# Optimization experiments

Measured on AMD Instinct MI355X. Metric: run time of the kernel, lower is better.

The kernel has to match this reference:

```python
import jax, jax.numpy as jnp
import numpy as np

B, S, H, J, LAT, OBS = 256, 128, 1024, 12, 64, 51
NL = 13                  # fk_model link count
PD = (NL + 1) * 3        # pos_dim = 42
FPS = 30.0
ACT_SCALE = 0.25
SMIN, SMAX = 0.05, 0.5
PIN = 2 * J + OBS + LAT  # 139


def setup_inputs() -> dict:
    key = jax.random.key(0)
    ks = jax.random.split(key, 16)
    rn = lambda k, shape, s=0.02: jax.random.normal(k, shape, dtype=jnp.float32) * s
    return dict(
        z=jax.random.normal(ks[0], (B, LAT), jnp.float32),
        obs_seq=jax.random.normal(ks[1], (B, S, OBS), jnp.float32),
        W1=rn(ks[2], (H, PIN)), b1=jnp.zeros((H,), jnp.float32),
        g1=jnp.ones((H,), jnp.float32), be1=jnp.zeros((H,), jnp.float32),
        W2=rn(ks[3], (H, H)), b2=jnp.zeros((H,), jnp.float32),
        g2=jnp.ones((H,), jnp.float32), be2=jnp.zeros((H,), jnp.float32),
        Wa1=rn(ks[4], (H, H)), ba1=jnp.zeros((H,), jnp.float32),
        Wa2=rn(ks[5], (J, H)), ba2=jnp.zeros((J,), jnp.float32),
        Wo=rn(ks[6], (3, H)), bo=jnp.zeros((3,), jnp.float32),
        Wv=rn(ks[7], (PD, H)), bv=jnp.full((PD,), -2.0, jnp.float32),  # torch init: zeros weight, bias=-2 (we keep small random W for non-degenerate grads)
        alpha_logits=jnp.full((J,), float(np.log(0.3)), jnp.float32),
        fk_W=rn(ks[8], (NL * 3, J), 0.1), fk_b=rn(ks[9], (NL * 3,), 0.1),  # linear FK surrogate
        pos_mean=rn(ks[10], (NL + 1, 3), 0.1),
        pos_std=1.0 + jax.random.uniform(ks[11], (NL + 1, 3), jnp.float32),
        joint_lower=jnp.full((J,), -2.0, jnp.float32),
        joint_upper=jnp.full((J,), 2.0, jnp.float32),
        default_dof_pos=rn(ks[12], (J,), 0.3),
    )


def _layernorm(x, g, b):
    m = jnp.mean(x, axis=-1, keepdims=True)
    v = jnp.var(x, axis=-1, keepdims=True)
    return (x - m) * jax.lax.rsqrt(v + 1e-5) * g + b


def reference(z, obs_seq, W1, b1, g1, be1, W2, b2, g2, be2, Wa1, ba1, Wa2, ba2,
              Wo, bo, Wv, bv, alpha_logits, fk_W, fk_b, pos_mean, pos_std,
              joint_lower, joint_upper, default_dof_pos):
    j_range = (joint_upper - joint_lower) / 2.0
    j_mean = (joint_upper + joint_lower) / 2.0
    alpha = jax.nn.sigmoid(alpha_logits)
    Bsz = z.shape[0]

    def step(carry, obs_t):
        pj, pdq = carry                                 # [B,J] each
        jn = (pj - j_mean) / j_range
        x = jnp.concatenate([jn, pdq, obs_t, z], axis=-1)   # [B,PIN]
        h = jax.nn.relu(_layernorm(x @ W1.T + b1, g1, be1))
        h = jax.nn.relu(_layernorm(h @ W2.T + b2, g2, be2))  # [B,H]
        a = jnp.tanh(jax.nn.relu(h @ Wa1.T + ba1) @ Wa2.T + ba2)  # [B,J]
        tgt = a * ACT_SCALE + default_dof_pos
        cj = jnp.clip(pj + alpha * (tgt - pj), joint_lower, joint_upper)
        obj = h @ Wo.T + bo                             # [B,3]
        # torch detaches the carried state (prev_joints/prev_dq)
        cdq = (cj - pj) * FPS
        new_carry = (jax.lax.stop_gradient(cj), jax.lax.stop_gradient(cdq))
        return new_carry, (h, a, cj, obj)

    pj0 = jnp.broadcast_to(default_dof_pos, (Bsz, J))
    pdq0 = jnp.zeros((Bsz, J), z.dtype)
    _, (hs, acts, joints, objs) = jax.lax.scan(step, (pj0, pdq0), jnp.swapaxes(obs_seq, 0, 1))

    features_seq = jnp.swapaxes(hs, 0, 1)    # [B,S,H]
    actions_seq = jnp.swapaxes(acts, 0, 1)   # [B,S,J]
    joint_traj = jnp.swapaxes(joints, 0, 1)  # [B,S,J]
    object_traj = jnp.swapaxes(objs, 0, 1)   # [B,S,3]

    agent_traj = joint_traj @ fk_W.T + fk_b  # [B,S,NL*3] linear FK surrogate
    combined = jnp.concatenate([agent_traj, object_traj], axis=-1)
    combined = combined.reshape(Bsz, S, NL + 1, 3)
    graph_x_mu = ((combined - pos_mean) / pos_std).reshape(Bsz, S, -1)  # [B,S,PD]

    sigma = SMIN + (SMAX - SMIN) * jax.nn.sigmoid(features_seq @ Wv.T + bv)
    log_sigma_pos = jnp.log(sigma)           # [B,S,PD]
    return (graph_x_mu, joint_traj, actions_seq, log_sigma_pos)
```

## Files before the change

kernel.cpp:

```cpp
#include <hip/hip_runtime.h>
#include <math.h>


#define NB 256
#define NS 128
#define NH 1024
#define NJ 12
#define NPIN 139
#define NPD 42
#define WPG 32
#define BROW 32
#define W2S 1032
#define AS 1032

typedef __attribute__((ext_vector_type(8))) short short8;
typedef __attribute__((ext_vector_type(4))) float f32x4;
typedef __attribute__((ext_vector_type(4))) unsigned short u16x4;

struct Params {
  const float* z; const float* obs; const float* W1; const float* b1;
  const float* g1; const float* be1; const float* W2; const float* b2;
  const float* g2; const float* be2; const float* Wa1; const float* ba1;
  const float* Wa2; const float* ba2; const float* Wo; const float* bo;
  const float* Wv; const float* bv; const float* alog; const float* fkW;
  const float* fkb; const float* pmean; const float* pstd; const float* jlo;
  const float* jhi; const float* ddp;
  float* out_gmu; float* out_joint; float* out_act; float* out_ls;
  float* zc; float* pa;
  unsigned short* y1b; unsigned short* y2b;
  unsigned short* wa1b; unsigned short* wexb;
  unsigned int* gcnt; unsigned int* slots;
};

__device__ __forceinline__ unsigned short f2bf(float x) {
  union { float f; unsigned u; } v; v.f = x;
  unsigned r = v.u + 0x7FFFu + ((v.u >> 16) & 1u);
  return (unsigned short)(r >> 16);
}
__device__ __forceinline__ float bf2f(unsigned short x) {
  union { unsigned u; float f; } v; v.u = ((unsigned)x) << 16;
  return v.f;
}
__device__ __forceinline__ unsigned cvt_pk_bf16(float lo, float hi) {
  unsigned r;
  asm("v_cvt_pk_bf16_f32 %0, %1, %2" : "=v"(r) : "v"(lo), "v"(hi));
  return r;
}
__device__ __forceinline__ void ld16_sc0(const unsigned short* p, short8& d) {
  asm volatile("global_load_dwordx4 %0, %1, off sc0" : "=v"(d) : "v"(p));
}
__device__ __forceinline__ void ldf4_sc0(const float* p, f32x4& d) {
  asm volatile("global_load_dwordx4 %0, %1, off sc0" : "=v"(d) : "v"(p));
}
__device__ __forceinline__ void vwait0() {
  asm volatile("s_waitcnt vmcnt(0)" ::: "memory");
  __builtin_amdgcn_sched_barrier(0);
}

__device__ __forceinline__ f32x4 dot1024(const unsigned short* a, const unsigned short* b) {
  const short8* ap = (const short8*)a;
  const short8* bp = (const short8*)b;
  f32x4 acc0 = {0.f, 0.f, 0.f, 0.f};
  f32x4 acc1 = {0.f, 0.f, 0.f, 0.f};
#pragma unroll 4
  for (int k8 = 0; k8 < 128; k8 += 8) {
    acc0 = __builtin_amdgcn_mfma_f32_16x16x32_bf16(ap[k8], bp[k8], acc0, 0, 0, 0);
    acc1 = __builtin_amdgcn_mfma_f32_16x16x32_bf16(ap[k8 + 4], bp[k8 + 4], acc1, 0, 0, 0);
  }
  return acc0 + acc1;
}

__device__ __forceinline__ void gbar(unsigned int* c, unsigned int target) {
  __threadfence();
  __syncthreads();
  if (threadIdx.x == 0) {
    __hip_atomic_fetch_add(c, 1u, __ATOMIC_RELEASE, __HIP_MEMORY_SCOPE_AGENT);
    unsigned long long t0 = __builtin_amdgcn_s_memrealtime();
    while (__hip_atomic_load(c, __ATOMIC_ACQUIRE, __HIP_MEMORY_SCOPE_AGENT) < target) {
      __builtin_amdgcn_s_sleep(16);
      if (__builtin_amdgcn_s_memrealtime() - t0 > (1ull << 25)) break;
    }
  }
  __syncthreads();
  __threadfence();
}

__device__ __forceinline__ void xbar2(unsigned int* sg, int w, unsigned target,
                                      int wave, int lane) {
  asm volatile("s_waitcnt vmcnt(0)" ::: "memory");
  __syncthreads();
  if (wave == 0) {
    if (lane == 0)
      __hip_atomic_fetch_add(sg + (size_t)w * 16, 1u, __ATOMIC_RELAXED,
                             __HIP_MEMORY_SCOPE_AGENT);
    const unsigned int* myslot = sg + (size_t)(lane & 31) * 16;
    unsigned long long t0 = __builtin_amdgcn_s_memrealtime();
    for (;;) {
      unsigned v;
      asm volatile("global_load_dword %0, %1, off sc0 sc1\n\t"
                   "s_waitcnt vmcnt(0)"
                   : "=v"(v) : "v"(myslot) : "memory");
      if (__all(v >= target)) break;
      __builtin_amdgcn_s_sleep(1);
      if (__builtin_amdgcn_s_memrealtime() - t0 > (1ull << 23)) break;
    }
  }
  __syncthreads();
}

__global__ __launch_bounds__(256, 1) void decoder_persistent(Params p) {
  __shared__ unsigned short w2l[BROW * W2S];
  __shared__ unsigned short albuf[BROW * AS];
  __shared__ float g1l[NH], be1l[NH], g2l[NH], be2l[NH];
  __shared__ unsigned short t1l[BROW * 40];
  __shared__ unsigned short wa2l[16 * 40];
  __shared__ float pj_l[BROW * NJ], pdq_l[BROW * NJ];
  __shared__ float alpha_l[NJ], jm_l[NJ], jri_l[NJ], lo_l[NJ], hi_l[NJ], ddp_l[NJ], ba2_l[NJ];
  __shared__ float pm_l[NPD], psi_l[NPD], bv_l[NPD], bo_l[4];

  const int tid = threadIdx.x;
  const int bid = blockIdx.x;
  const int g = bid & 7;
  const int w = bid >> 3;
  const int b0 = g * BROW;
  const int n0 = w * 32;
  const int wave = tid >> 6;
  const int lane = tid & 63;

  unsigned int* sg = p.slots + (size_t)g * 512;
  unsigned short* y1bg = p.y1b + (size_t)g * BROW * NH;
  unsigned short* y2bg = p.y2b + (size_t)g * BROW * NH;
  float* pa_gg = p.pa + (size_t)g * BROW * NJ * 32;

  if (tid < NJ) {
    alpha_l[tid] = 1.f / (1.f + expf(-p.alog[tid]));
    float lo = p.jlo[tid], hi = p.jhi[tid];
    jm_l[tid] = 0.5f * (hi + lo);
    jri_l[tid] = 2.f / (hi - lo);
    lo_l[tid] = lo; hi_l[tid] = hi;
    ddp_l[tid] = p.ddp[tid]; ba2_l[tid] = p.ba2[tid];
  }
  if (tid < NPD) { pm_l[tid] = p.pmean[tid]; psi_l[tid] = 1.f / p.pstd[tid]; bv_l[tid] = p.bv[tid]; }
  if (tid < 3) bo_l[tid] = p.bo[tid];
  for (int idx = tid; idx < BROW * NJ; idx += 256) { pj_l[idx] = p.ddp[idx % NJ]; pdq_l[idx] = 0.f; }
  for (int idx = tid; idx < NH; idx += 256) {
    g1l[idx] = p.g1[idx]; be1l[idx] = p.be1[idx];
    g2l[idx] = p.g2[idx]; be2l[idx] = p.be2[idx];
  }
  for (int idx = tid; idx < BROW * NH; idx += 256) {
    int r = idx >> 10, k = idx & (NH - 1);
    w2l[r * W2S + k] = f2bf(p.W2[(size_t)(n0 + r) * NH + k]);
  }
  for (int idx = tid; idx < 16 * 32; idx += 256) {
    int rr = idx >> 5, cc = idx & 31;
    wa2l[rr * 40 + cc] = (rr < NJ) ? f2bf(p.Wa2[(size_t)rr * NH + n0 + cc]) : (unsigned short)0;
  }
  {
    int r = tid >> 3, cq = tid & 7;
    int nb = n0 + cq * 4;
    const float* zr = p.z + (size_t)(b0 + r) * 64;
    const float* w1r = p.W1 + (size_t)nb * NPIN + 75;
    float a0 = p.b1[nb], a1 = p.b1[nb + 1], a2 = p.b1[nb + 2], a3 = p.b1[nb + 3];
    for (int k = 0; k < 64; ++k) {
      float zv = zr[k];
      a0 += zv * w1r[k]; a1 += zv * w1r[NPIN + k];
      a2 += zv * w1r[2 * NPIN + k]; a3 += zv * w1r[3 * NPIN + k];
    }
    f32x4 st = {a0, a1, a2, a3};
    *(f32x4*)(p.zc + (size_t)(b0 + r) * NH + nb) = st;
  }
  for (int idx = tid; idx < 4 * NH; idx += 256) {
    int r = idx >> 10, k = idx & (NH - 1);
    int row = n0 + g * 4 + r;
    p.wa1b[(size_t)row * NH + k] = f2bf(p.Wa1[(size_t)row * NH + k]);
  }
  if (bid == 1) {
    for (int idx = tid; idx < 48 * NH; idx += 256) {
      int r = idx >> 10, k = idx & (NH - 1);
      unsigned short v = 0;
      if (r < 3) v = f2bf(p.Wo[(size_t)r * NH + k]);
      else if (r < 45) v = f2bf(p.Wv[(size_t)(r - 3) * NH + k]);
      p.wexb[idx] = v;
    }
  }
  gbar(p.gcnt, 256u);

  auto stage_ln = [&](const unsigned short* yg, const float* gl, const float* bl) {
    const int r = tid >> 3, cq = tid & 7;
    const unsigned short* src = yg + (size_t)r * NH + cq * 8;
    unsigned short* dst = &albuf[r * AS + cq * 8];
    short8 v[16];
#pragma unroll
    for (int i = 0; i < 16; ++i) ld16_sc0(src + (size_t)i * 64, v[i]);
    vwait0();
    float s = 0.f, q = 0.f;
#pragma unroll
    for (int i = 0; i < 16; ++i)
#pragma unroll
      for (int jj = 0; jj < 8; ++jj) {
        float x = bf2f((unsigned short)v[i][jj]);
        s += x; q = fmaf(x, x, q);
      }
#pragma unroll
    for (int off = 4; off; off >>= 1) {
      s += __shfl_down(s, off, 8);
      q += __shfl_down(q, off, 8);
    }
    s = __shfl(s, 0, 8); q = __shfl(q, 0, 8);
    float m = s * (1.f / 1024.f);
    float rs = rsqrtf(q * (1.f / 1024.f) - m * m + 1e-5f);
    float nmrs = -m * rs;
#pragma unroll
    for (int i = 0; i < 16; ++i) {
      int c = cq * 8 + i * 64;
      f32x4 ga = *(const f32x4*)(gl + c);
      f32x4 gb = *(const f32x4*)(gl + c + 4);
      f32x4 ba = *(const f32x4*)(bl + c);
      f32x4 bb = *(const f32x4*)(bl + c + 4);
      float xn[8];
#pragma unroll
      for (int jj = 0; jj < 8; ++jj) {
        float x = bf2f((unsigned short)v[i][jj]);
        float tn = fmaf(x, rs, nmrs);
        float gg = (jj < 4) ? ga[jj] : gb[jj - 4];
        float bv2 = (jj < 4) ? ba[jj] : bb[jj - 4];
        xn[jj] = fmaxf(fmaf(tn, gg, bv2), 0.f);
      }
      uint4 pk = {cvt_pk_bf16(xn[0], xn[1]), cvt_pk_bf16(xn[2], xn[3]),
                  cvt_pk_bf16(xn[4], xn[5]), cvt_pk_bf16(xn[6], xn[7])};
      *(uint4*)(dst + i * 64) = pk;
    }
  };

  auto P1 = [&](int t) {
    int r = tid >> 3, cq = tid & 7;
    int nb = n0 + cq * 4;
    float xj[24];
#pragma unroll
    for (int j = 0; j < NJ; ++j) {
      xj[j] = (pj_l[r * NJ + j] - jm_l[j]) * jri_l[j];
      xj[12 + j] = pdq_l[r * NJ + j];
    }
    f32x4 acc = *(const f32x4*)(p.zc + (size_t)(b0 + r) * NH + nb);
    const float* w1r = p.W1 + (size_t)nb * NPIN;
#pragma unroll
    for (int k = 0; k < 24; ++k) {
      float xv = xj[k];
      acc[0] += xv * w1r[k]; acc[1] += xv * w1r[NPIN + k];
      acc[2] += xv * w1r[2 * NPIN + k]; acc[3] += xv * w1r[3 * NPIN + k];
    }
    const float* ob = p.obs + ((size_t)(b0 + r) * NS + t) * 51;
    for (int o = 0; o < 51; ++o) {
      float ov = ob[o];
      acc[0] += ov * w1r[24 + o]; acc[1] += ov * w1r[NPIN + 24 + o];
      acc[2] += ov * w1r[2 * NPIN + 24 + o]; acc[3] += ov * w1r[3 * NPIN + 24 + o];
    }
    u16x4 hv = {f2bf(acc[0]), f2bf(acc[1]), f2bf(acc[2]), f2bf(acc[3])};
    *(u16x4*)(y1bg + (size_t)r * NH + nb) = hv;
  };

  auto Yphase = [&]() {
    stage_ln(y1bg, g1l, be1l);
    __syncthreads();
    int rt = wave >> 1, ct = wave & 1;
    int kq = (lane >> 4) * 8;
    const unsigned short* a = &albuf[(rt * 16 + (lane & 15)) * AS + kq];
    const unsigned short* b = &w2l[(ct * 16 + (lane & 15)) * W2S + kq];
    f32x4 acc = dot1024(a, b);
    int col = n0 + ct * 16 + (lane & 15);
    float b2v = p.b2[col];
#pragma unroll
    for (int i = 0; i < 4; ++i) {
      int row = rt * 16 + (lane >> 4) * 4 + i;
      y2bg[(size_t)row * NH + col] = f2bf(acc[i] + b2v);
    }
  };

  auto Zphase = [&](int t) {
    stage_ln(y2bg, g2l, be2l);
    __syncthreads();
    int rt = wave >> 1, ct = wave & 1;
    int kq = (lane >> 4) * 8;
    {
      const unsigned short* a = &albuf[(rt * 16 + (lane & 15)) * AS + kq];
      const unsigned short* b = p.wa1b + (size_t)(n0 + ct * 16 + (lane & 15)) * NH + kq;
      f32x4 acc = dot1024(a, b);
      int lcol = ct * 16 + (lane & 15);
      float bav = p.ba1[n0 + lcol];
#pragma unroll
      for (int i = 0; i < 4; ++i) {
        int row = rt * 16 + (lane >> 4) * 4 + i;
        t1l[row * 40 + lcol] = f2bf(fmaxf(acc[i] + bav, 0.f));
      }
    }
    __syncthreads();
    if (wave < 2) {
      int k0 = (lane >> 4) * 8;
      short8 a8 = *(const short8*)&t1l[(wave * 16 + (lane & 15)) * 40 + k0];
      short8 b8 = *(const short8*)&wa2l[(lane & 15) * 40 + k0];
      f32x4 z4 = {0.f, 0.f, 0.f, 0.f};
      f32x4 d = __builtin_amdgcn_mfma_f32_16x16x32_bf16(a8, b8, z4, 0, 0, 0);
      int j = lane & 15;
      if (j < NJ) {
#pragma unroll
        for (int i = 0; i < 4; ++i) {
          int row = wave * 16 + (lane >> 4) * 4 + i;
          pa_gg[((size_t)row * NJ + j) * 32 + w] = d[i];
        }
      }
    }
    if (w >= 26 && wave == 3) {
      int e = w - 26, cte = e >> 1, rte = e & 1;
      const unsigned short* a = &albuf[(rte * 16 + (lane & 15)) * AS + kq];
      const unsigned short* b = p.wexb + (size_t)(cte * 16 + (lane & 15)) * NH + kq;
      f32x4 acc = dot1024(a, b);
      int ec = cte * 16 + (lane & 15);
#pragma unroll
      for (int i = 0; i < 4; ++i) {
        int row = rte * 16 + (lane >> 4) * 4 + i;
        int bb = b0 + row;
        if (ec < 3) {
          float val = acc[i] + bo_l[ec];
          p.out_gmu[((size_t)bb * NS + t) * NPD + 39 + ec] = (val - pm_l[39 + ec]) * psi_l[39 + ec];
        } else if (ec < 45) {
          int sv = ec - 3;
          float val = acc[i] + bv_l[sv];
          float sig = 0.05f + 0.45f / (1.f + expf(-val));
          p.out_ls[((size_t)bb * NS + t) * NPD + sv] = logf(sig);
        }
      }
    }
  };

  auto Xmid = [&](int tp) {
    for (int e = tid; e < BROW * NJ; e += 256) {
      const float* pp = pa_gg + (size_t)e * 32;
      f32x4 u[8];
#pragma unroll
      for (int c2 = 0; c2 < 8; ++c2) ldf4_sc0(pp + c2 * 4, u[c2]);
      vwait0();
      f32x4 ss = ((u[0] + u[1]) + (u[2] + u[3])) + ((u[4] + u[5]) + (u[6] + u[7]));
      float sum = ss[0] + ss[1] + ss[2] + ss[3];
      int r = e / NJ, j = e - r * NJ;
      float av = tanhf(sum + ba2_l[j]);
      float pj = pj_l[e];
      float tgt = av * 0.25f + ddp_l[j];
      float cj = pj + alpha_l[j] * (tgt - pj);
      cj = fminf(fmaxf(cj, lo_l[j]), hi_l[j]);
      pdq_l[e] = (cj - pj) * 30.f;
      pj_l[e] = cj;
      if (w == 0) {
        size_t o = ((size_t)(b0 + r) * NS + tp) * NJ + j;
        p.out_joint[o] = cj;
        p.out_act[o] = av;
      }
    }
    __syncthreads();
    if (w == 0) {
      for (int idx = tid; idx < BROW * 39; idx += 256) {
        int r = idx / 39, m = idx - r * 39;
        float s = p.fkb[m];
        const float* fw = p.fkW + m * NJ;
#pragma unroll
        for (int j = 0; j < NJ; ++j) s += pj_l[r * NJ + j] * fw[j];
        p.out_gmu[((size_t)(b0 + r) * NS + tp) * NPD + m] = (s - pm_l[m]) * psi_l[m];
      }
    }
  };

  unsigned int nbar = 0;
  for (int t = 0; t < NS; ++t) {
    if (t > 0) Xmid(t - 1);
    P1(t);
    xbar2(sg, w, ++nbar, wave, lane);
    Yphase();
    xbar2(sg, w, ++nbar, wave, lane);
    Zphase(t);
    xbar2(sg, w, ++nbar, wave, lane);
  }
  Xmid(NS - 1);
}

extern "C" void kernel_launch(void* const* d_in, const int* in_sizes, int n_in,
                              void* d_out, int out_size, void* d_ws, size_t ws_size,
                              hipStream_t stream) {
  (void)in_sizes; (void)n_in; (void)out_size; (void)ws_size;
  char* ws = (char*)d_ws;
  Params p;
  p.z = (const float*)d_in[0];   p.obs = (const float*)d_in[1];
  p.W1 = (const float*)d_in[2];  p.b1 = (const float*)d_in[3];
  p.g1 = (const float*)d_in[4];  p.be1 = (const float*)d_in[5];
  p.W2 = (const float*)d_in[6];  p.b2 = (const float*)d_in[7];
  p.g2 = (const float*)d_in[8];  p.be2 = (const float*)d_in[9];
  p.Wa1 = (const float*)d_in[10]; p.ba1 = (const float*)d_in[11];
  p.Wa2 = (const float*)d_in[12]; p.ba2 = (const float*)d_in[13];
  p.Wo = (const float*)d_in[14]; p.bo = (const float*)d_in[15];
  p.Wv = (const float*)d_in[16]; p.bv = (const float*)d_in[17];
  p.alog = (const float*)d_in[18];
  p.fkW = (const float*)d_in[19]; p.fkb = (const float*)d_in[20];
  p.pmean = (const float*)d_in[21]; p.pstd = (const float*)d_in[22];
  p.jlo = (const float*)d_in[23]; p.jhi = (const float*)d_in[24];
  p.ddp = (const float*)d_in[25];

  float* out = (float*)d_out;
  p.out_gmu = out;
  p.out_joint = out + (size_t)256 * 128 * 42;
  p.out_act = p.out_joint + (size_t)256 * 128 * 12;
  p.out_ls = p.out_act + (size_t)256 * 128 * 12;

  p.gcnt = (unsigned int*)(ws + 0);
  p.slots = (unsigned int*)(ws + 1024);
  size_t off = (size_t)1 << 15;
  p.zc = (float*)(ws + off);                 off += (size_t)NB * NH * 4;
  p.y1b = (unsigned short*)(ws + off);       off += (size_t)NB * NH * 2;
  p.y2b = (unsigned short*)(ws + off);       off += (size_t)NB * NH * 2;
  p.pa = (float*)(ws + off);                 off += (size_t)8 * 32 * 12 * 32 * 4;
  p.wa1b = (unsigned short*)(ws + off);      off += (size_t)NH * NH * 2;
  p.wexb = (unsigned short*)(ws + off);

  hipMemsetAsync(d_ws, 0, 1 << 15, stream);
  decoder_persistent<<<dim3(256), dim3(256), 0, stream>>>(p);
}
```

Baseline: 3.873 ms.

## Fuse LayerNorm partial stats into producers and overlap obs projection with barrier

Producers of y1 and y2 now compute per-row partial sums and sums of squares and write them to small global buffers. The LayerNorm staging then reduces these partials instead of re-reading every bf16 value for the statistics. The loop is also restructured so the observation part of the first-layer projection for the next step is issued between the barrier arrive and the wait, hiding it behind synchronisation latency. The cost is extra global writes and reads of partials and a more intricate barrier schedule. Statistics are computed from fp32 values before bf16 rounding, which changes numerics slightly.

```diff
diff --git a/kernel.cpp b/kernel.cpp
--- a/kernel.cpp
+++ b/kernel.cpp
@@ -26,7 +26,7 @@
   const float* fkb; const float* pmean; const float* pstd; const float* jlo;
   const float* jhi; const float* ddp;
   float* out_gmu; float* out_joint; float* out_act; float* out_ls;
-  float* zc; float* pa;
+  float* zc; float* pa; float* part1; float* part2;
   unsigned short* y1b; unsigned short* y2b;
   unsigned short* wa1b; unsigned short* wexb;
   unsigned int* gcnt; unsigned int* slots;
@@ -85,6 +85,20 @@
   __threadfence();
 }
 
+__device__ __forceinline__ void slot_wait(unsigned int* sg, unsigned target, int lane) {
+  const unsigned int* myslot = sg + (size_t)(lane & 31) * 16;
+  unsigned long long t0 = __builtin_amdgcn_s_memrealtime();
+  for (;;) {
+    unsigned v;
+    asm volatile("global_load_dword %0, %1, off sc0 sc1\n\t"
+                 "s_waitcnt vmcnt(0)"
+                 : "=v"(v) : "v"(myslot) : "memory");
+    if (__all(v >= target)) break;
+    __builtin_amdgcn_s_sleep(1);
+    if (__builtin_amdgcn_s_memrealtime() - t0 > (1ull << 23)) break;
+  }
+}
+
 __device__ __forceinline__ void xbar2(unsigned int* sg, int w, unsigned target,
                                       int wave, int lane) {
   asm volatile("s_waitcnt vmcnt(0)" ::: "memory");
@@ -93,17 +107,7 @@
     if (lane == 0)
       __hip_atomic_fetch_add(sg + (size_t)w * 16, 1u, __ATOMIC_RELAXED,
                              __HIP_MEMORY_SCOPE_AGENT);
-    const unsigned int* myslot = sg + (size_t)(lane & 31) * 16;
-    unsigned long long t0 = __builtin_amdgcn_s_memrealtime();
-    for (;;) {
-      unsigned v;
-      asm volatile("global_load_dword %0, %1, off sc0 sc1\n\t"
-                   "s_waitcnt vmcnt(0)"
-                   : "=v"(v) : "v"(myslot) : "memory");
-      if (__all(v >= target)) break;
-      __builtin_amdgcn_s_sleep(1);
-      if (__builtin_amdgcn_s_memrealtime() - t0 > (1ull << 23)) break;
-    }
+    slot_wait(sg, target, lane);
   }
   __syncthreads();
 }
@@ -131,6 +135,8 @@
   unsigned short* y1bg = p.y1b + (size_t)g * BROW * NH;
   unsigned short* y2bg = p.y2b + (size_t)g * BROW * NH;
   float* pa_gg = p.pa + (size_t)g * BROW * NJ * 32;
+  float* part1g = p.part1 + (size_t)g * BROW * 64;
+  float* part2g = p.part2 + (size_t)g * BROW * 128;
 
   if (tid < NJ) {
     alpha_l[tid] = 1.f / (1.f + expf(-p.alog[tid]));
@@ -185,22 +191,27 @@
   }
   gbar(p.gcnt, 256u);
 
-  auto stage_ln = [&](const unsigned short* yg, const float* gl, const float* bl) {
+  auto stage_ln_apply = [&](const unsigned short* yg, const float* part, bool wide,
+                            const float* gl, const float* bl) {
     const int r = tid >> 3, cq = tid & 7;
     const unsigned short* src = yg + (size_t)r * NH + cq * 8;
     unsigned short* dst = &albuf[r * AS + cq * 8];
     short8 v[16];
 #pragma unroll
     for (int i = 0; i < 16; ++i) ld16_sc0(src + (size_t)i * 64, v[i]);
+    const int fpr = wide ? 128 : 64;
+    const float* pp = part + (size_t)r * fpr + cq * (fpr >> 3);
+    f32x4 p0, p1, p2 = {0, 0, 0, 0}, p3 = {0, 0, 0, 0};
+    ldf4_sc0(pp, p0);
+    ldf4_sc0(pp + 4, p1);
+    if (wide) { ldf4_sc0(pp + 8, p2); ldf4_sc0(pp + 12, p3); }
     vwait0();
-    float s = 0.f, q = 0.f;
-#pragma unroll
-    for (int i = 0; i < 16; ++i)
-#pragma unroll
-      for (int jj = 0; jj < 8; ++jj) {
-        float x = bf2f((unsigned short)v[i][jj]);
-        s += x; q = fmaf(x, x, q);
-      }
+    float s = p0[0] + p0[2] + p1[0] + p1[2];
+    float q = p0[1] + p0[3] + p1[1] + p1[3];
+    if (wide) {
+      s += p2[0] + p2[2] + p3[0] + p3[2];
+      q += p2[1] + p2[3] + p3[1] + p3[3];
+    }
 #pragma unroll
     for (int off = 4; off; off >>= 1) {
       s += __shfl_down(s, off, 8);
@@ -232,35 +243,52 @@
     }
   };
 
-  auto P1 = [&](int t) {
+  auto P1_obs = [&](int t) -> f32x4 {
     int r = tid >> 3, cq = tid & 7;
     int nb = n0 + cq * 4;
-    float xj[24];
-#pragma unroll
-    for (int j = 0; j < NJ; ++j) {
-      xj[j] = (pj_l[r * NJ + j] - jm_l[j]) * jri_l[j];
-      xj[12 + j] = pdq_l[r * NJ + j];
-    }
     f32x4 acc = *(const f32x4*)(p.zc + (size_t)(b0 + r) * NH + nb);
     const float* w1r = p.W1 + (size_t)nb * NPIN;
-#pragma unroll
-    for (int k = 0; k < 24; ++k) {
-      float xv = xj[k];
-      acc[0] += xv * w1r[k]; acc[1] += xv * w1r[NPIN + k];
-      acc[2] += xv * w1r[2 * NPIN + k]; acc[3] += xv * w1r[3 * NPIN + k];
-    }
     const float* ob = p.obs + ((size_t)(b0 + r) * NS + t) * 51;
     for (int o = 0; o < 51; ++o) {
       float ov = ob[o];
       acc[0] += ov * w1r[24 + o]; acc[1] += ov * w1r[NPIN + 24 + o];
       acc[2] += ov * w1r[2 * NPIN + 24 + o]; acc[3] += ov * w1r[3 * NPIN + 24 + o];
     }
+    return acc;
+  };
+  auto P1_fin = [&](f32x4 acc) {
+    int r = tid >> 3, cq = tid & 7;
+    int nb = n0 + cq * 4;
+    float xj[24];
+#pragma unroll
+    for (int j = 0; j < NJ; ++j) {
+      xj[j] = (pj_l[r * NJ + j] - jm_l[j]) * jri_l[j];
+      xj[12 + j] = pdq_l[r * NJ + j];
+    }
+    const float* w1r = p.W1 + (size_t)nb * NPIN;
+#pragma unroll
+    for (int k = 0; k < 24; ++k) {
+      float xv = xj[k];
+      acc[0] += xv * w1r[k]; acc[1] += xv * w1r[NPIN + k];
+      acc[2] += xv * w1r[2 * NPIN + k]; acc[3] += xv * w1r[3 * NPIN + k];
+    }
     u16x4 hv = {f2bf(acc[0]), f2bf(acc[1]), f2bf(acc[2]), f2bf(acc[3])};
     *(u16x4*)(y1bg + (size_t)r * NH + nb) = hv;
+    float s = acc[0] + acc[1] + acc[2] + acc[3];
+    float q = acc[0] * acc[0] + acc[1] * acc[1] + acc[2] * acc[2] + acc[3] * acc[3];
+#pragma unroll
+    for (int off = 4; off; off >>= 1) {
+      s += __shfl_down(s, off, 8);
+      q += __shfl_down(q, off, 8);
+    }
+    if ((tid & 7) == 0) {
+      float* pw = part1g + (size_t)r * 64 + w * 2;
+      pw[0] = s; pw[1] = q;
+    }
   };
 
   auto Yphase = [&]() {
-    stage_ln(y1bg, g1l, be1l);
+    stage_ln_apply(y1bg, part1g, false, g1l, be1l);
     __syncthreads();
     int rt = wave >> 1, ct = wave & 1;
     int kq = (lane >> 4) * 8;
@@ -269,15 +297,34 @@
     f32x4 acc = dot1024(a, b);
     int col = n0 + ct * 16 + (lane & 15);
     float b2v = p.b2[col];
+    float sv[4], qv[4];
 #pragma unroll
     for (int i = 0; i < 4; ++i) {
       int row = rt * 16 + (lane >> 4) * 4 + i;
-      y2bg[(size_t)row * NH + col] = f2bf(acc[i] + b2v);
+      float val = acc[i] + b2v;
+      y2bg[(size_t)row * NH + col] = f2bf(val);
+      sv[i] = val; qv[i] = val * val;
+    }
+#pragma unroll
+    for (int mask = 1; mask < 16; mask <<= 1) {
+#pragma unroll
+      for (int i = 0; i < 4; ++i) {
+        sv[i] += __shfl_xor(sv[i], mask, 64);
+        qv[i] += __shfl_xor(qv[i], mask, 64);
+      }
+    }
+    if ((lane & 15) == 0) {
+      int rbase = rt * 16 + (lane >> 4) * 4;
+#pragma unroll
+      for (int i = 0; i < 4; ++i) {
+        float* pw = part2g + (size_t)(rbase + i) * 128 + (w * 2 + ct) * 2;
+        pw[0] = sv[i]; pw[1] = qv[i];
+      }
     }
   };
 
   auto Zphase = [&](int t) {
-    stage_ln(y2bg, g2l, be2l);
+    stage_ln_apply(y2bg, part2g, true, g2l, be2l);
     __syncthreads();
     int rt = wave >> 1, ct = wave & 1;
     int kq = (lane >> 4) * 8;
@@ -323,10 +370,10 @@
           float val = acc[i] + bo_l[ec];
           p.out_gmu[((size_t)bb * NS + t) * NPD + 39 + ec] = (val - pm_l[39 + ec]) * psi_l[39 + ec];
         } else if (ec < 45) {
-          int sv = ec - 3;
-          float val = acc[i] + bv_l[sv];
+          int sv2 = ec - 3;
+          float val = acc[i] + bv_l[sv2];
           float sig = 0.05f + 0.45f / (1.f + expf(-val));
-          p.out_ls[((size_t)bb * NS + t) * NPD + sv] = logf(sig);
+          p.out_ls[((size_t)bb * NS + t) * NPD + sv2] = logf(sig);
         }
       }
     }
@@ -368,17 +415,32 @@
     }
   };
 
-  unsigned int nbar = 0;
+  unsigned nbar = 0;
+  {
+    f32x4 acc = P1_obs(0);
+    P1_fin(acc);
+    xbar2(sg, w, ++nbar, wave, lane);
+  }
   for (int t = 0; t < NS; ++t) {
-    if (t > 0) Xmid(t - 1);
-    P1(t);
-    xbar2(sg, w, ++nbar, wave, lane);
     Yphase();
     xbar2(sg, w, ++nbar, wave, lane);
     Zphase(t);
-    xbar2(sg, w, ++nbar, wave, lane);
-  }
-  Xmid(NS - 1);
+    unsigned tc = ++nbar;
+    asm volatile("s_waitcnt vmcnt(0)" ::: "memory");
+    __syncthreads();
+    if (tid == 0)
+      __hip_atomic_fetch_add(sg + (size_t)w * 16, 1u, __ATOMIC_RELAXED,
+                             __HIP_MEMORY_SCOPE_AGENT);
+    f32x4 acc = {0.f, 0.f, 0.f, 0.f};
+    if (t + 1 < NS) acc = P1_obs(t + 1);
+    if (wave == 0) slot_wait(sg, tc, lane);
+    __syncthreads();
+    Xmid(t);
+    if (t + 1 < NS) {
+      P1_fin(acc);
+      xbar2(sg, w, ++nbar, wave, lane);
+    }
+  }
 }
 
 extern "C" void kernel_launch(void* const* d_in, const int* in_sizes, int n_in,
@@ -415,6 +477,8 @@
   p.y1b = (unsigned short*)(ws + off);       off += (size_t)NB * NH * 2;
   p.y2b = (unsigned short*)(ws + off);       off += (size_t)NB * NH * 2;
   p.pa = (float*)(ws + off);                 off += (size_t)8 * 32 * 12 * 32 * 4;
+  p.part1 = (float*)(ws + off);              off += (size_t)8 * 32 * 64 * 4;
+  p.part2 = (float*)(ws + off);              off += (size_t)8 * 32 * 128 * 4;
   p.wa1b = (unsigned short*)(ws + off);      off += (size_t)NH * NH * 2;
   p.wexb = (unsigned short*)(ws + off);
 
```

Measured after the change: 3.673 ms. -5.2%, faster.

## Split batch group into two half-tiles with split arrive/wait barriers and partial LN stats

Applied to the files above, without the earlier changes.

Each 32-row batch group is split into two 16-row halves with separate barrier slot sets. Each barrier becomes an arrive followed by a later wait, so one half's phase can overlap the other half's barrier latency. Producers now write per-row partial sum and sum-of-squares, so the layernorm staging reads 16 columns' partials instead of recomputing statistics over the full row. This doubles the barrier count and halves the MFMA tile per phase, which leaves waves idle, in exchange for hiding cross-block synchronisation latency.

```diff
diff --git a/kernel.cpp b/kernel.cpp
--- a/kernel.cpp
+++ b/kernel.cpp
@@ -15,7 +15,7 @@
 
 typedef __attribute__((ext_vector_type(8))) short short8;
 typedef __attribute__((ext_vector_type(4))) float f32x4;
-typedef __attribute__((ext_vector_type(4))) unsigned short u16x4;
+typedef __attribute__((ext_vector_type(2))) float f32x2;
 
 struct Params {
   const float* z; const float* obs; const float* W1; const float* b1;
@@ -26,7 +26,7 @@
   const float* fkb; const float* pmean; const float* pstd; const float* jlo;
   const float* jhi; const float* ddp;
   float* out_gmu; float* out_joint; float* out_act; float* out_ls;
-  float* zc; float* pa;
+  float* zc; float* pa; float* part1; float* part2;
   unsigned short* y1b; unsigned short* y2b;
   unsigned short* wa1b; unsigned short* wexb;
   unsigned int* gcnt; unsigned int* slots;
@@ -85,36 +85,38 @@
   __threadfence();
 }
 
-__device__ __forceinline__ void xbar2(unsigned int* sg, int w, unsigned target,
-                                      int wave, int lane) {
+__device__ __forceinline__ void slot_wait(const unsigned int* sg, unsigned target, int lane) {
+  const unsigned int* myslot = sg + (size_t)(lane & 31) * 16;
+  unsigned long long t0 = __builtin_amdgcn_s_memrealtime();
+  for (;;) {
+    unsigned v;
+    asm volatile("global_load_dword %0, %1, off sc0 sc1\n\t"
+                 "s_waitcnt vmcnt(0)"
+                 : "=v"(v) : "v"(myslot) : "memory");
+    if (__all(v >= target)) break;
+    __builtin_amdgcn_s_sleep(1);
+    if (__builtin_amdgcn_s_memrealtime() - t0 > (1ull << 23)) break;
+  }
+}
+__device__ __forceinline__ void arrive_bar(unsigned int* myslot, int tid) {
   asm volatile("s_waitcnt vmcnt(0)" ::: "memory");
   __syncthreads();
-  if (wave == 0) {
-    if (lane == 0)
-      __hip_atomic_fetch_add(sg + (size_t)w * 16, 1u, __ATOMIC_RELAXED,
-                             __HIP_MEMORY_SCOPE_AGENT);
-    const unsigned int* myslot = sg + (size_t)(lane & 31) * 16;
-    unsigned long long t0 = __builtin_amdgcn_s_memrealtime();
-    for (;;) {
-      unsigned v;
-      asm volatile("global_load_dword %0, %1, off sc0 sc1\n\t"
-                   "s_waitcnt vmcnt(0)"
-                   : "=v"(v) : "v"(myslot) : "memory");
-      if (__all(v >= target)) break;
-      __builtin_amdgcn_s_sleep(1);
-      if (__builtin_amdgcn_s_memrealtime() - t0 > (1ull << 23)) break;
-    }
-  }
+  if (tid == 0)
+    __hip_atomic_fetch_add(myslot, 1u, __ATOMIC_RELAXED, __HIP_MEMORY_SCOPE_AGENT);
+}
+__device__ __forceinline__ void wait_bar(const unsigned int* sg, unsigned target,
+                                         int wave, int lane) {
+  if (wave == 0) slot_wait(sg, target, lane);
   __syncthreads();
 }
 
 __global__ __launch_bounds__(256, 1) void decoder_persistent(Params p) {
   __shared__ unsigned short w2l[BROW * W2S];
-  __shared__ unsigned short albuf[BROW * AS];
+  __shared__ unsigned short albuf[16 * AS];
   __shared__ float g1l[NH], be1l[NH], g2l[NH], be2l[NH];
-  __shared__ unsigned short t1l[BROW * 40];
+  __shared__ unsigned short t1l[16 * 40];
   __shared__ unsigned short wa2l[16 * 40];
-  __shared__ float pj_l[BROW * NJ], pdq_l[BROW * NJ];
+  __shared__ float pjA[16 * NJ], pdqA[16 * NJ], pjB[16 * NJ], pdqB[16 * NJ];
   __shared__ float alpha_l[NJ], jm_l[NJ], jri_l[NJ], lo_l[NJ], hi_l[NJ], ddp_l[NJ], ba2_l[NJ];
   __shared__ float pm_l[NPD], psi_l[NPD], bv_l[NPD], bo_l[4];
 
@@ -127,10 +129,16 @@
   const int wave = tid >> 6;
   const int lane = tid & 63;
 
-  unsigned int* sg = p.slots + (size_t)g * 512;
+  unsigned int* sgA = p.slots + (size_t)(g * 2 + 0) * 512;
+  unsigned int* sgB = p.slots + (size_t)(g * 2 + 1) * 512;
+  unsigned int* arrA = sgA + (size_t)w * 16;
+  unsigned int* arrB = sgB + (size_t)w * 16;
+
   unsigned short* y1bg = p.y1b + (size_t)g * BROW * NH;
   unsigned short* y2bg = p.y2b + (size_t)g * BROW * NH;
   float* pa_gg = p.pa + (size_t)g * BROW * NJ * 32;
+  float* part1g = p.part1 + (size_t)g * BROW * 64;
+  float* part2g = p.part2 + (size_t)g * BROW * 128;
 
   if (tid < NJ) {
     alpha_l[tid] = 1.f / (1.f + expf(-p.alog[tid]));
@@ -142,7 +150,10 @@
   }
   if (tid < NPD) { pm_l[tid] = p.pmean[tid]; psi_l[tid] = 1.f / p.pstd[tid]; bv_l[tid] = p.bv[tid]; }
   if (tid < 3) bo_l[tid] = p.bo[tid];
-  for (int idx = tid; idx < BROW * NJ; idx += 256) { pj_l[idx] = p.ddp[idx % NJ]; pdq_l[idx] = 0.f; }
+  if (tid < 16 * NJ) {
+    pjA[tid] = p.ddp[tid % NJ]; pdqA[tid] = 0.f;
+    pjB[tid] = p.ddp[tid % NJ]; pdqB[tid] = 0.f;
+  }
   for (int idx = tid; idx < NH; idx += 256) {
     g1l[idx] = p.g1[idx]; be1l[idx] = p.be1[idx];
     g2l[idx] = p.g2[idx]; be2l[idx] = p.be2[idx];
@@ -185,34 +196,38 @@
   }
   gbar(p.gcnt, 256u);
 
-  auto stage_ln = [&](const unsigned short* yg, const float* gl, const float* bl) {
-    const int r = tid >> 3, cq = tid & 7;
-    const unsigned short* src = yg + (size_t)r * NH + cq * 8;
-    unsigned short* dst = &albuf[r * AS + cq * 8];
-    short8 v[16];
-#pragma unroll
-    for (int i = 0; i < 16; ++i) ld16_sc0(src + (size_t)i * 64, v[i]);
+  auto stage_ln = [&](int h, const unsigned short* yg, const float* part, bool wide,
+                      const float* gl, const float* bl) {
+    const int r = tid >> 4, cl = tid & 15;
+    const int hofs = h * 16;
+    const unsigned short* src = yg + (size_t)(hofs + r) * NH + cl * 8;
+    unsigned short* dst = &albuf[r * AS + cl * 8];
+    short8 v[8];
+#pragma unroll
+    for (int i = 0; i < 8; ++i) ld16_sc0(src + (size_t)i * 128, v[i]);
+    f32x4 q0, q1 = {0, 0, 0, 0};
+    if (wide) {
+      const float* pp = part + (size_t)(hofs + r) * 128 + cl * 8;
+      ldf4_sc0(pp, q0); ldf4_sc0(pp + 4, q1);
+    } else {
+      const float* pp = part + (size_t)(hofs + r) * 64 + cl * 4;
+      ldf4_sc0(pp, q0);
+    }
     vwait0();
-    float s = 0.f, q = 0.f;
-#pragma unroll
-    for (int i = 0; i < 16; ++i)
-#pragma unroll
-      for (int jj = 0; jj < 8; ++jj) {
-        float x = bf2f((unsigned short)v[i][jj]);
-        s += x; q = fmaf(x, x, q);
-      }
-#pragma unroll
-    for (int off = 4; off; off >>= 1) {
-      s += __shfl_down(s, off, 8);
-      q += __shfl_down(q, off, 8);
-    }
-    s = __shfl(s, 0, 8); q = __shfl(q, 0, 8);
+    float s = q0[0] + q0[2] + q1[0] + q1[2];
+    float q = q0[1] + q0[3] + q1[1] + q1[3];
+#pragma unroll
+    for (int off = 8; off; off >>= 1) {
+      s += __shfl_down(s, off, 16);
+      q += __shfl_down(q, off, 16);
+    }
+    s = __shfl(s, 0, 16); q = __shfl(q, 0, 16);
     float m = s * (1.f / 1024.f);
     float rs = rsqrtf(q * (1.f / 1024.f) - m * m + 1e-5f);
     float nmrs = -m * rs;
 #pragma unroll
-    for (int i = 0; i < 16; ++i) {
-      int c = cq * 8 + i * 64;
+    for (int i = 0; i < 8; ++i) {
+      int c = cl * 8 + i * 128;
       f32x4 ga = *(const f32x4*)(gl + c);
       f32x4 gb = *(const f32x4*)(gl + c + 4);
       f32x4 ba = *(const f32x4*)(bl + c);
@@ -228,75 +243,107 @@
       }
       uint4 pk = {cvt_pk_bf16(xn[0], xn[1]), cvt_pk_bf16(xn[2], xn[3]),
                   cvt_pk_bf16(xn[4], xn[5]), cvt_pk_bf16(xn[6], xn[7])};
-      *(uint4*)(dst + i * 64) = pk;
+      *(uint4*)(dst + i * 128) = pk;
     }
   };
 
-  auto P1 = [&](int t) {
-    int r = tid >> 3, cq = tid & 7;
-    int nb = n0 + cq * 4;
-    float xj[24];
-#pragma unroll
-    for (int j = 0; j < NJ; ++j) {
-      xj[j] = (pj_l[r * NJ + j] - jm_l[j]) * jri_l[j];
-      xj[12 + j] = pdq_l[r * NJ + j];
-    }
-    f32x4 acc = *(const f32x4*)(p.zc + (size_t)(b0 + r) * NH + nb);
-    const float* w1r = p.W1 + (size_t)nb * NPIN;
-#pragma unroll
-    for (int k = 0; k < 24; ++k) {
-      float xv = xj[k];
-      acc[0] += xv * w1r[k]; acc[1] += xv * w1r[NPIN + k];
-      acc[2] += xv * w1r[2 * NPIN + k]; acc[3] += xv * w1r[3 * NPIN + k];
-    }
-    const float* ob = p.obs + ((size_t)(b0 + r) * NS + t) * 51;
+  auto P1 = [&](int h, int t) {
+    const int r = tid >> 4, cl = tid & 15;
+    const int nb = n0 + cl * 2;
+    const int grow = b0 + h * 16 + r;
+    const float* pj = h ? pjB : pjA;
+    const float* pdq = h ? pdqB : pdqA;
+    const float* zrow = p.zc + (size_t)grow * NH;
+    float a0 = zrow[nb], a1 = zrow[nb + 1];
+    const float* w0 = p.W1 + (size_t)nb * NPIN;
+    const float* w1p = w0 + NPIN;
+    const float* ob = p.obs + ((size_t)grow * NS + t) * 51;
     for (int o = 0; o < 51; ++o) {
       float ov = ob[o];
-      acc[0] += ov * w1r[24 + o]; acc[1] += ov * w1r[NPIN + 24 + o];
-      acc[2] += ov * w1r[2 * NPIN + 24 + o]; acc[3] += ov * w1r[3 * NPIN + 24 + o];
-    }
-    u16x4 hv = {f2bf(acc[0]), f2bf(acc[1]), f2bf(acc[2]), f2bf(acc[3])};
-    *(u16x4*)(y1bg + (size_t)r * NH + nb) = hv;
+      a0 += ov * w0[24 + o]; a1 += ov * w1p[24 + o];
+    }
+    float xj[24];
+#pragma unroll
+    for (int j = 0; j < NJ; ++j) {
+      xj[j] = (pj[r * NJ + j] - jm_l[j]) * jri_l[j];
+      xj[12 + j] = pdq[r * NJ + j];
+    }
+#pragma unroll
+    for (int k = 0; k < 24; ++k) {
+      a0 += xj[k] * w0[k]; a1 += xj[k] * w1p[k];
+    }
+    *(unsigned*)(y1bg + (size_t)(h * 16 + r) * NH + nb) = cvt_pk_bf16(a0, a1);
+    float s = a0 + a1, q = a0 * a0 + a1 * a1;
+#pragma unroll
+    for (int off = 8; off; off >>= 1) {
+      s += __shfl_down(s, off, 16);
+      q += __shfl_down(q, off, 16);
+    }
+    if (cl == 0) {
+      f32x2 pw = {s, q};
+      *(f32x2*)(part1g + (size_t)(h * 16 + r) * 64 + w * 2) = pw;
+    }
   };
 
-  auto Yphase = [&]() {
-    stage_ln(y1bg, g1l, be1l);
+  auto Yph = [&](int h) {
+    stage_ln(h, y1bg, part1g, false, g1l, be1l);
     __syncthreads();
-    int rt = wave >> 1, ct = wave & 1;
-    int kq = (lane >> 4) * 8;
-    const unsigned short* a = &albuf[(rt * 16 + (lane & 15)) * AS + kq];
-    const unsigned short* b = &w2l[(ct * 16 + (lane & 15)) * W2S + kq];
-    f32x4 acc = dot1024(a, b);
-    int col = n0 + ct * 16 + (lane & 15);
-    float b2v = p.b2[col];
-#pragma unroll
-    for (int i = 0; i < 4; ++i) {
-      int row = rt * 16 + (lane >> 4) * 4 + i;
-      y2bg[(size_t)row * NH + col] = f2bf(acc[i] + b2v);
+    if (wave < 2) {
+      const int ct = wave;
+      const int kq = (lane >> 4) * 8;
+      const unsigned short* a = &albuf[(lane & 15) * AS + kq];
+      const unsigned short* b = &w2l[(ct * 16 + (lane & 15)) * W2S + kq];
+      f32x4 acc = dot1024(a, b);
+      int col = n0 + ct * 16 + (lane & 15);
+      float b2v = p.b2[col];
+      float sv[4], qv[4];
+#pragma unroll
+      for (int i = 0; i < 4; ++i) {
+        int row = (lane >> 4) * 4 + i;
+        float val = acc[i] + b2v;
+        y2bg[(size_t)(h * 16 + row) * NH + col] = f2bf(val);
+        sv[i] = val; qv[i] = val * val;
+      }
+#pragma unroll
+      for (int mask = 1; mask < 16; mask <<= 1) {
+#pragma unroll
+        for (int i = 0; i < 4; ++i) {
+          sv[i] += __shfl_xor(sv[i], mask, 64);
+          qv[i] += __shfl_xor(qv[i], mask, 64);
+        }
+      }
+      if ((lane & 15) == 0) {
+        int rbase = (lane >> 4) * 4;
+#pragma unroll
+        for (int i = 0; i < 4; ++i) {
+          f32x2 pw = {sv[i], qv[i]};
+          *(f32x2*)(part2g + (size_t)(h * 16 + rbase + i) * 128 + (w * 2 + ct) * 2) = pw;
+        }
+      }
     }
   };
 
-  auto Zphase = [&](int t) {
-    stage_ln(y2bg, g2l, be2l);
+  auto Zph = [&](int h, int t) {
+    stage_ln(h, y2bg, part2g, true, g2l, be2l);
     __syncthreads();
-    int rt = wave >> 1, ct = wave & 1;
-    int kq = (lane >> 4) * 8;
-    {
-      const unsigned short* a = &albuf[(rt * 16 + (lane & 15)) * AS + kq];
+    if (wave < 2) {
+      const int ct = wave;
+      const int kq = (lane >> 4) * 8;
+      const unsigned short* a = &albuf[(lane & 15) * AS + kq];
       const unsigned short* b = p.wa1b + (size_t)(n0 + ct * 16 + (lane & 15)) * NH + kq;
       f32x4 acc = dot1024(a, b);
       int lcol = ct * 16 + (lane & 15);
       float bav = p.ba1[n0 + lcol];
 #pragma unroll
       for (int i = 0; i < 4; ++i) {
-        int row = rt * 16 + (lane >> 4) * 4 + i;
+        int row = (lane >> 4) * 4 + i;
         t1l[row * 40 + lcol] = f2bf(fmaxf(acc[i] + bav, 0.f));
       }
     }
     __syncthreads();
-    if (wave < 2) {
+    if (wave == 0) {
       int k0 = (lane >> 4) * 8;
-      short8 a8 = *(const short8*)&t1l[(wave * 16 + (lane & 15)) * 40 + k0];
+      short8 a8 = *(const short8*)&t1l[(lane & 15) * 40 + k0];
       short8 b8 = *(const short8*)&wa2l[(lane & 15) * 40 + k0];
       f32x4 z4 = {0.f, 0.f, 0.f, 0.f};
       f32x4 d = __builtin_amdgcn_mfma_f32_16x16x32_bf16(a8, b8, z4, 0, 0, 0);
@@ -304,37 +351,41 @@
       if (j < NJ) {
 #pragma unroll
         for (int i = 0; i < 4; ++i) {
-          int row = wave * 16 + (lane >> 4) * 4 + i;
-          pa_gg[((size_t)row * NJ + j) * 32 + w] = d[i];
+          int row = (lane >> 4) * 4 + i;
+          pa_gg[((size_t)(h * 16 + row) * NJ + j) * 32 + w] = d[i];
         }
       }
     }
-    if (w >= 26 && wave == 3) {
-      int e = w - 26, cte = e >> 1, rte = e & 1;
-      const unsigned short* a = &albuf[(rte * 16 + (lane & 15)) * AS + kq];
+    if (wave == 3 && w >= 26 + 3 * h && w < 29 + 3 * h) {
+      const int cte = w - (26 + 3 * h);
+      const int kq = (lane >> 4) * 8;
+      const unsigned short* a = &albuf[(lane & 15) * AS + kq];
       const unsigned short* b = p.wexb + (size_t)(cte * 16 + (lane & 15)) * NH + kq;
       f32x4 acc = dot1024(a, b);
       int ec = cte * 16 + (lane & 15);
 #pragma unroll
       for (int i = 0; i < 4; ++i) {
-        int row = rte * 16 + (lane >> 4) * 4 + i;
-        int bb = b0 + row;
+        int row = (lane >> 4) * 4 + i;
+        int bb = b0 + h * 16 + row;
         if (ec < 3) {
           float val = acc[i] + bo_l[ec];
           p.out_gmu[((size_t)bb * NS + t) * NPD + 39 + ec] = (val - pm_l[39 + ec]) * psi_l[39 + ec];
         } else if (ec < 45) {
-          int sv = ec - 3;
-          float val = acc[i] + bv_l[sv];
+          int sv2 = ec - 3;
+          float val = acc[i] + bv_l[sv2];
           float sig = 0.05f + 0.45f / (1.f + expf(-val));
-          p.out_ls[((size_t)bb * NS + t) * NPD + sv] = logf(sig);
+          p.out_ls[((size_t)bb * NS + t) * NPD + sv2] = logf(sig);
         }
       }
     }
   };
 
-  auto Xmid = [&](int tp) {
-    for (int e = tid; e < BROW * NJ; e += 256) {
-      const float* pp = pa_gg + (size_t)e * 32;
+  auto Xph = [&](int h, int tp) {
+    float* pj = h ? pjB : pjA;
+    float* pdq = h ? pdqB : pdqA;
+    if (tid < 16 * NJ) {
+      const int e = tid;
+      const float* pp = pa_gg + ((size_t)h * 16 * NJ + e) * 32;
       f32x4 u[8];
 #pragma unroll
       for (int c2 = 0; c2 < 8; ++c2) ldf4_sc0(pp + c2 * 4, u[c2]);
@@ -343,42 +394,50 @@
       float sum = ss[0] + ss[1] + ss[2] + ss[3];
       int r = e / NJ, j = e - r * NJ;
       float av = tanhf(sum + ba2_l[j]);
-      float pj = pj_l[e];
+      float old = pj[e];
       float tgt = av * 0.25f + ddp_l[j];
-      float cj = pj + alpha_l[j] * (tgt - pj);
+      float cj = old + alpha_l[j] * (tgt - old);
       cj = fminf(fmaxf(cj, lo_l[j]), hi_l[j]);
-      pdq_l[e] = (cj - pj) * 30.f;
-      pj_l[e] = cj;
+      pdq[e] = (cj - old) * 30.f;
+      pj[e] = cj;
       if (w == 0) {
-        size_t o = ((size_t)(b0 + r) * NS + tp) * NJ + j;
+        size_t o = ((size_t)(b0 + h * 16 + r) * NS + tp) * NJ + j;
         p.out_joint[o] = cj;
         p.out_act[o] = av;
       }
     }
     __syncthreads();
     if (w == 0) {
-      for (int idx = tid; idx < BROW * 39; idx += 256) {
+      for (int idx = tid; idx < 16 * 39; idx += 256) {
         int r = idx / 39, m = idx - r * 39;
         float s = p.fkb[m];
         const float* fw = p.fkW + m * NJ;
 #pragma unroll
-        for (int j = 0; j < NJ; ++j) s += pj_l[r * NJ + j] * fw[j];
-        p.out_gmu[((size_t)(b0 + r) * NS + tp) * NPD + m] = (s - pm_l[m]) * psi_l[m];
+        for (int j = 0; j < NJ; ++j) s += pj[r * NJ + j] * fw[j];
+        p.out_gmu[((size_t)(b0 + h * 16 + r) * NS + tp) * NPD + m] = (s - pm_l[m]) * psi_l[m];
       }
     }
   };
 
-  unsigned int nbar = 0;
+  unsigned nbA = 0, nbB = 0;
+  P1(0, 0); arrive_bar(arrA, tid); ++nbA;
+  P1(1, 0); arrive_bar(arrB, tid); ++nbB;
   for (int t = 0; t < NS; ++t) {
-    if (t > 0) Xmid(t - 1);
-    P1(t);
-    xbar2(sg, w, ++nbar, wave, lane);
-    Yphase();
-    xbar2(sg, w, ++nbar, wave, lane);
-    Zphase(t);
-    xbar2(sg, w, ++nbar, wave, lane);
-  }
-  Xmid(NS - 1);
+    wait_bar(sgA, nbA, wave, lane);
+    Yph(0);  arrive_bar(arrA, tid); ++nbA;
+    wait_bar(sgB, nbB, wave, lane);
+    Yph(1);  arrive_bar(arrB, tid); ++nbB;
+    wait_bar(sgA, nbA, wave, lane);
+    Zph(0, t); arrive_bar(arrA, tid); ++nbA;
+    wait_bar(sgB, nbB, wave, lane);
+    Zph(1, t); arrive_bar(arrB, tid); ++nbB;
+    wait_bar(sgA, nbA, wave, lane);
+    Xph(0, t);
+    if (t + 1 < NS) { P1(0, t + 1); arrive_bar(arrA, tid); ++nbA; }
+    wait_bar(sgB, nbB, wave, lane);
+    Xph(1, t);
+    if (t + 1 < NS) { P1(1, t + 1); arrive_bar(arrB, tid); ++nbB; }
+  }
 }
 
 extern "C" void kernel_launch(void* const* d_in, const int* in_sizes, int n_in,
@@ -410,14 +469,16 @@
 
   p.gcnt = (unsigned int*)(ws + 0);
   p.slots = (unsigned int*)(ws + 1024);
-  size_t off = (size_t)1 << 15;
+  size_t off = (size_t)1 << 16;
   p.zc = (float*)(ws + off);                 off += (size_t)NB * NH * 4;
   p.y1b = (unsigned short*)(ws + off);       off += (size_t)NB * NH * 2;
   p.y2b = (unsigned short*)(ws + off);       off += (size_t)NB * NH * 2;
   p.pa = (float*)(ws + off);                 off += (size_t)8 * 32 * 12 * 32 * 4;
+  p.part1 = (float*)(ws + off);              off += (size_t)8 * 32 * 64 * 4;
+  p.part2 = (float*)(ws + off);              off += (size_t)8 * 32 * 128 * 4;
   p.wa1b = (unsigned short*)(ws + off);      off += (size_t)NH * NH * 2;
   p.wexb = (unsigned short*)(ws + off);
 
-  hipMemsetAsync(d_ws, 0, 1 << 15, stream);
+  hipMemsetAsync(d_ws, 0, 1 << 16, stream);
   decoder_persistent<<<dim3(256), dim3(256), 0, stream>>>(p);
 }
```

Result: slower. 4.705 ms (+21.5%).
